# Kernel optimization log

Hardware: AMD Instinct MI355X
Metric: run time of the kernel (lower is better)

## Reference

```python
import jax, jax.numpy as jnp
import numpy as np

B, E, H, NC = 16384, 1024, 8, 32
FF = 4 * E

def _ln(x, g, b, eps=1e-5):
    m = jnp.mean(x, -1, keepdims=True)
    v = jnp.mean((x - m) ** 2, -1, keepdims=True)
    return (x - m) * jax.lax.rsqrt(v + eps) * g + b

def _mha1(q_in, kv_in, Wq, Wk, Wv, bq, bk, bv, Wo, bo):
    # seq_len == 1 for both query and key/value; x: [B, E]
    Bn = q_in.shape[0]
    dh = E // H
    q = (q_in @ Wq.T + bq).reshape(Bn, H, dh)
    k = (kv_in @ Wk.T + bk).reshape(Bn, H, dh)
    v = (kv_in @ Wv.T + bv).reshape(Bn, H, dh)
    s = jnp.sum(q * k, -1, keepdims=True) / np.float32(np.sqrt(dh))  # [B,H,1]
    w = jax.nn.softmax(s, axis=-1)  # single key -> weights == 1 exactly
    o = (w * v).reshape(Bn, E)
    return o @ Wo.T + bo

def _ffn(x, W1, b1, W2, b2):
    h = jax.nn.gelu(x @ W1.T + b1, approximate=False)  # torch GELU = exact erf
    return h @ W2.T + b2

def setup_inputs():
    key = jax.random.key(0)
    ks = iter(jax.random.split(key, 64))
    def w(shape, s=0.02):
        return jax.random.normal(next(ks), shape, jnp.float32) * s
    z = lambda n: jnp.zeros((n,), jnp.float32)
    o = lambda n: jnp.ones((n,), jnp.float32)
    d = {
        'lc_cls': jax.random.normal(next(ks), (B, E), jnp.float32),
        'tab_embedding': jax.random.normal(next(ks), (B, E), jnp.float32),
        'ln_lc_g': o(E), 'ln_lc_b': z(E),
        'ln_tab_g': o(E), 'ln_tab_b': z(E),
    }
    for p in ('alc', 'atab'):
        d[p + '_Wq'] = w((E, E)); d[p + '_Wk'] = w((E, E)); d[p + '_Wv'] = w((E, E))
        d[p + '_bq'] = z(E); d[p + '_bk'] = z(E); d[p + '_bv'] = z(E)
        d[p + '_Wo'] = w((E, E)); d[p + '_bo'] = z(E)
    for p in ('flc', 'ftab'):
        d[p + '_W1'] = w((FF, E)); d[p + '_b1'] = z(FF)
        d[p + '_W2'] = w((E, FF)); d[p + '_b2'] = z(E)
    d['on_g'] = o(2 * E); d['on_b'] = z(2 * E)
    d['c_W1'] = w((E, 2 * E)); d['c_b1'] = z(E)
    d['c_ln_g'] = o(E); d['c_ln_b'] = z(E)
    d['c_W2'] = w((NC, E)); d['c_b2'] = z(NC)
    return d

def reference(lc_cls, tab_embedding, ln_lc_g, ln_lc_b, ln_tab_g, ln_tab_b,
              alc_Wq, alc_Wk, alc_Wv, alc_bq, alc_bk, alc_bv, alc_Wo, alc_bo,
              atab_Wq, atab_Wk, atab_Wv, atab_bq, atab_bk, atab_bv, atab_Wo, atab_bo,
              flc_W1, flc_b1, flc_W2, flc_b2, ftab_W1, ftab_b1, ftab_W2, ftab_b2,
              on_g, on_b, c_W1, c_b1, c_ln_g, c_ln_b, c_W2, c_b2):
    # dropout is identity at inference
    lc_n = _ln(lc_cls, ln_lc_g, ln_lc_b)
    tab_n = _ln(tab_embedding, ln_tab_g, ln_tab_b)
    lc_cross = lc_cls + _mha1(lc_n, tab_n, alc_Wq, alc_Wk, alc_Wv, alc_bq, alc_bk, alc_bv, alc_Wo, alc_bo)
    tab_cross = tab_embedding + _mha1(tab_n, lc_n, atab_Wq, atab_Wk, atab_Wv, atab_bq, atab_bk, atab_bv, atab_Wo, atab_bo)
    lc_out = lc_cross + _ffn(lc_cross, flc_W1, flc_b1, flc_W2, flc_b2)
    tab_out = tab_cross + _ffn(tab_cross, ftab_W1, ftab_b1, ftab_W2, ftab_b2)
    fused = _ln(jnp.concatenate([lc_out, tab_out], axis=1), on_g, on_b)
    h = jax.nn.gelu(_ln(fused @ c_W1.T + c_b1, c_ln_g, c_ln_b), approximate=False)
    return h @ c_W2.T + c_b2
```

## Files before the change

kernel.cpp:

```cpp
#include <hip/hip_runtime.h>
#include <hip/hip_bf16.h>
#include <math.h>

typedef __bf16 bf16_t;
typedef __bf16 bf16x8 __attribute__((ext_vector_type(8)));
typedef __bf16 bf16x4 __attribute__((ext_vector_type(4)));
typedef float  f32x4  __attribute__((ext_vector_type(4)));

#define NB   16384
#define EDIM 1024
#define FFD  4096
#define NCD  32

__device__ __forceinline__ float gelu_exact(float x) {
    return 0.5f * x * (1.0f + erff(x * 0.70710678118654752f));
}

__device__ __forceinline__ void gload16(const bf16_t* g, bf16_t* l) {
    __builtin_amdgcn_global_load_lds(
        (__attribute__((address_space(1))) void*)(g),
        (__attribute__((address_space(3))) void*)(l),
        16, 0, 0);
}

#define PH_BAR() do { asm volatile("" ::: "memory"); \
                      __builtin_amdgcn_s_barrier();  \
                      asm volatile("" ::: "memory"); } while (0)

enum { EPI_PLAIN = 0, EPI_RESF32 = 1, EPI_GELU = 2, EPI_RESBF16 = 3 };

struct GemmArgs {
    const bf16_t* A0; const bf16_t* A1;
    const bf16_t* B0; const bf16_t* B1;
    const float*  bias0; const float* bias1;
    const void*   res0; const void*  res1;
    bf16_t*       out0; bf16_t*      out1;
};

template<int EPI>
__global__ __launch_bounds__(512, 4)
void gemmP2(GemmArgs g, int ldo, int co0, int co1, int M, int N, int K)
{
    __shared__ __align__(128) bf16_t lds[36864];
    char* const ldsb = (char*)lds;

    const int nx   = gridDim.x;
    const int ny   = M >> 8;
    const int nwg  = nx * gridDim.y;
    const int lin  = blockIdx.y * nx + blockIdx.x;
    const int Wx   = nwg >> 3;
    const int w    = (lin & 7) * Wx + (lin >> 3);
    const int perSide = nx * ny;
    const int side = w / perSide;
    const int r    = w - side * perSide;
    const int cg   = r / (ny << 3);
    const int tt   = r - cg * (ny << 3);
    const long bm  = (long)(tt >> 3) * 256;
    const long bn  = (long)((cg << 3) + (tt & 7)) * 128;

    const bf16_t* __restrict__ A    = side ? g.A1   : g.A0;
    const bf16_t* __restrict__ Bw   = side ? g.B1   : g.B0;
    const float*  __restrict__ bias = side ? g.bias1: g.bias0;
    const void*   __restrict__ resid= side ? g.res1 : g.res0;
    bf16_t*       __restrict__ out  = side ? g.out1 : g.out0;
    const int coloff = side ? co1 : co0;

    const int tid = threadIdx.x, lane = tid & 63, wave = tid >> 6;
    const int wm = wave >> 1, wn = wave & 1;
    const int fr = lane & 15, ks = lane >> 4;
    const int csw = ((ks ^ (fr & 3)) << 4);

    const int sl = ((tid & 3) ^ ((tid >> 2) & 3)) * 8;
    const bf16_t* gA = A  + (bm + (tid >> 2)) * (long)K + sl;
    const bf16_t* gB = Bw + (bn + (tid >> 2)) * (long)K + sl;
    bf16_t* const dA0 = (bf16_t*)(ldsb + wave * 1024);
    bf16_t* const dA1 = (bf16_t*)(ldsb + 8192  + wave * 1024);
    bf16_t* const dB  = (bf16_t*)(ldsb + 16384 + wave * 1024);

    const int nt = K >> 5;
    auto STAGE = [&](int t) {
        const int bufo = (t % 3) * 24576;
        const long kt = (long)t << 5;
        gload16(gA + kt,                 (bf16_t*)((char*)dA0 + bufo));
        gload16(gA + kt + 128 * (long)K, (bf16_t*)((char*)dA1 + bufo));
        gload16(gB + kt,                 (bf16_t*)((char*)dB  + bufo));
    };

    f32x4 acc[4][4] = {};

    STAGE(0);
    STAGE(1);
    asm volatile("s_waitcnt vmcnt(3)" ::: "memory");
    PH_BAR();

    for (int t = 0; t < nt; ++t) {
        const char* base = ldsb + (t % 3) * 24576;
        bf16x8 av[4], bv[4];
        #pragma unroll
        for (int i = 0; i < 4; ++i) {
            av[i] = *(const bf16x8*)(base + (wm * 64 + i * 16 + fr) * 64 + csw);
            bv[i] = *(const bf16x8*)(base + 16384 + (wn * 64 + i * 16 + fr) * 64 + csw);
        }
        if (t + 2 < nt) STAGE(t + 2);
        __builtin_amdgcn_s_setprio(1);
        #pragma unroll
        for (int mi = 0; mi < 4; ++mi)
            #pragma unroll
            for (int ni = 0; ni < 4; ++ni)
                acc[mi][ni] = __builtin_amdgcn_mfma_f32_16x16x32_bf16(
                                  av[mi], bv[ni], acc[mi][ni], 0, 0, 0);
        __builtin_amdgcn_s_setprio(0);
        if (t + 2 < nt) { asm volatile("s_waitcnt vmcnt(3)" ::: "memory"); }
        else            { asm volatile("s_waitcnt vmcnt(0)" ::: "memory"); }
        PH_BAR();
    }

    const int rq = (lane >> 4) * 4;
    #pragma unroll
    for (int mi = 0; mi < 4; ++mi) {
        #pragma unroll
        for (int ni = 0; ni < 4; ++ni) {
            const long n = bn + wn * 64 + ni * 16 + fr;
            const float bval = bias ? bias[n] : 0.0f;
            #pragma unroll
            for (int r2 = 0; r2 < 4; ++r2) {
                const long m = bm + wm * 64 + mi * 16 + rq + r2;
                float v = acc[mi][ni][r2] + bval;
                if (EPI == EPI_RESF32)  v += ((const float*)resid)[m * (long)N + n];
                if (EPI == EPI_RESBF16) v += (float)((const bf16_t*)resid)[m * (long)N + n];
                if (EPI == EPI_GELU)    v = gelu_exact(v);
                out[m * (long)ldo + coloff + n] = (bf16_t)v;
            }
        }
    }
}

__global__ __launch_bounds__(256)
void final_mfma(const bf16_t* __restrict__ U, const bf16_t* __restrict__ W2,
                const float* __restrict__ b2, float* __restrict__ out)
{
    __shared__ bf16_t sA[128 * 32];
    __shared__ bf16_t sB[32 * 32];
    const int tid = threadIdx.x, lane = tid & 63, wave = tid >> 6;
    const long bm = (long)blockIdx.x * 128;
    const int srow = lane >> 2, scol = (lane & 3) * 8;

    const bf16_t* gA = U + (bm + wave * 32 + srow) * (long)EDIM + scol;
    bf16_t* lA = sA + wave * 32 * 32;
    const bf16_t* gB = W2 + ((long)wave * 16 + srow) * EDIM + scol;
    bf16_t* lB = sB + wave * 16 * 32;

    const int fr = lane & 15, fk = (lane >> 4) * 8;
    const bf16_t* rA = sA + (wave * 32 + fr) * 32 + fk;
    const bf16_t* rB = sB + fr * 32 + fk;

    f32x4 acc[2][2] = {};
    for (int kt = 0; kt < EDIM; kt += 32) {
        gload16(gA + kt,             lA);
        gload16(gA + kt + 16 * EDIM, lA + 16 * 32);
        if (wave < 2) gload16(gB + kt, lB);
        __syncthreads();
        bf16x8 av[2], bv[2];
        av[0] = *(const bf16x8*)(rA);
        av[1] = *(const bf16x8*)(rA + 16 * 32);
        bv[0] = *(const bf16x8*)(rB);
        bv[1] = *(const bf16x8*)(rB + 16 * 32);
        #pragma unroll
        for (int mi = 0; mi < 2; ++mi)
            #pragma unroll
            for (int ni = 0; ni < 2; ++ni)
                acc[mi][ni] = __builtin_amdgcn_mfma_f32_16x16x32_bf16(
                                  av[mi], bv[ni], acc[mi][ni], 0, 0, 0);
        __syncthreads();
    }
    const int rq = (lane >> 4) * 4;
    #pragma unroll
    for (int mi = 0; mi < 2; ++mi)
        #pragma unroll
        for (int ni = 0; ni < 2; ++ni) {
            const int n = ni * 16 + fr;
            const float bval = b2[n];
            #pragma unroll
            for (int r = 0; r < 4; ++r) {
                const long m = bm + wave * 32 + mi * 16 + rq + r;
                out[m * NCD + n] = acc[mi][ni][r] + bval;
            }
        }
}

__global__ __launch_bounds__(256)
void ln_f32(const float* __restrict__ X, const float* __restrict__ g,
            const float* __restrict__ b, bf16_t* __restrict__ out)
{
    const long row = blockIdx.x;
    const int t = threadIdx.x;
    f32x4 x = ((const f32x4*)(X + row * EDIM))[t];
    float s = x[0] + x[1] + x[2] + x[3];
    float q = x[0]*x[0] + x[1]*x[1] + x[2]*x[2] + x[3]*x[3];
    #pragma unroll
    for (int off = 32; off; off >>= 1) { s += __shfl_xor(s, off); q += __shfl_xor(q, off); }
    __shared__ float red[8];
    if ((t & 63) == 0) { red[(t >> 6) * 2] = s; red[(t >> 6) * 2 + 1] = q; }
    __syncthreads();
    s = red[0] + red[2] + red[4] + red[6];
    q = red[1] + red[3] + red[5] + red[7];
    const float mean = s * (1.0f / EDIM);
    const float rs = rsqrtf(q * (1.0f / EDIM) - mean * mean + 1e-5f);
    f32x4 gg = ((const f32x4*)g)[t];
    f32x4 bb = ((const f32x4*)b)[t];
    bf16x4 o;
    #pragma unroll
    for (int j = 0; j < 4; ++j) o[j] = (bf16_t)((x[j] - mean) * rs * gg[j] + bb[j]);
    ((bf16x4*)(out + row * EDIM))[t] = o;
}

__global__ __launch_bounds__(256)
void ln_cat(const bf16_t* __restrict__ X, const float* __restrict__ g,
            const float* __restrict__ b, bf16_t* __restrict__ out)
{
    const long row = blockIdx.x;
    const int t = threadIdx.x;
    bf16x8 xv = ((const bf16x8*)(X + row * 2048))[t];
    float xf[8];
    float s = 0.f, q = 0.f;
    #pragma unroll
    for (int j = 0; j < 8; ++j) { xf[j] = (float)xv[j]; s += xf[j]; q += xf[j] * xf[j]; }
    #pragma unroll
    for (int off = 32; off; off >>= 1) { s += __shfl_xor(s, off); q += __shfl_xor(q, off); }
    __shared__ float red[8];
    if ((t & 63) == 0) { red[(t >> 6) * 2] = s; red[(t >> 6) * 2 + 1] = q; }
    __syncthreads();
    s = red[0] + red[2] + red[4] + red[6];
    q = red[1] + red[3] + red[5] + red[7];
    const float mean = s * (1.0f / 2048);
    const float rs = rsqrtf(q * (1.0f / 2048) - mean * mean + 1e-5f);
    f32x4 g0 = ((const f32x4*)g)[2 * t], g1 = ((const f32x4*)g)[2 * t + 1];
    f32x4 b0 = ((const f32x4*)b)[2 * t], b1 = ((const f32x4*)b)[2 * t + 1];
    bf16x8 o;
    #pragma unroll
    for (int j = 0; j < 4; ++j) o[j]     = (bf16_t)((xf[j]     - mean) * rs * g0[j] + b0[j]);
    #pragma unroll
    for (int j = 0; j < 4; ++j) o[4 + j] = (bf16_t)((xf[4 + j] - mean) * rs * g1[j] + b1[j]);
    ((bf16x8*)(out + row * 2048))[t] = o;
}

__global__ __launch_bounds__(256)
void ln_gelu(const bf16_t* __restrict__ X, const float* __restrict__ g,
             const float* __restrict__ b, bf16_t* __restrict__ out)
{
    const long row = blockIdx.x;
    const int t = threadIdx.x;
    bf16x4 xv = ((const bf16x4*)(X + row * EDIM))[t];
    float xf[4];
    float s = 0.f, q = 0.f;
    #pragma unroll
    for (int j = 0; j < 4; ++j) { xf[j] = (float)xv[j]; s += xf[j]; q += xf[j] * xf[j]; }
    #pragma unroll
    for (int off = 32; off; off >>= 1) { s += __shfl_xor(s, off); q += __shfl_xor(q, off); }
    __shared__ float red[8];
    if ((t & 63) == 0) { red[(t >> 6) * 2] = s; red[(t >> 6) * 2 + 1] = q; }
    __syncthreads();
    s = red[0] + red[2] + red[4] + red[6];
    q = red[1] + red[3] + red[5] + red[7];
    const float mean = s * (1.0f / EDIM);
    const float rs = rsqrtf(q * (1.0f / EDIM) - mean * mean + 1e-5f);
    f32x4 gg = ((const f32x4*)g)[t];
    f32x4 bb = ((const f32x4*)b)[t];
    bf16x4 o;
    #pragma unroll
    for (int j = 0; j < 4; ++j)
        o[j] = (bf16_t)gelu_exact((xf[j] - mean) * rs * gg[j] + bb[j]);
    ((bf16x4*)(out + row * EDIM))[t] = o;
}

__global__ void f2b(const float* __restrict__ in, bf16_t* __restrict__ out, long n4)
{
    long i = (long)blockIdx.x * blockDim.x + threadIdx.x;
    const long stride = (long)gridDim.x * blockDim.x;
    for (; i < n4; i += stride) {
        f32x4 v = ((const f32x4*)in)[i];
        bf16x4 o;
        #pragma unroll
        for (int j = 0; j < 4; ++j) o[j] = (bf16_t)v[j];
        ((bf16x4*)out)[i] = o;
    }
}

__global__ void tconv(const float* __restrict__ in, bf16_t* __restrict__ out)
{
    const long x = (long)blockIdx.x * 256 + threadIdx.x;
    const int k = (int)(x & (EDIM - 1));
    const int j = (int)(x >> 10);
    out[(long)j * EDIM + k] = (bf16_t)in[(long)k * EDIM + j];
}

__global__ __launch_bounds__(256)
void bcomb_k(const float* __restrict__ Wo, const float* __restrict__ bv,
             const float* __restrict__ bo, float* __restrict__ bc)
{
    const int i = blockIdx.x;
    const int t = threadIdx.x;
    f32x4 w = ((const f32x4*)(Wo + (long)i * EDIM))[t];
    f32x4 v = ((const f32x4*)bv)[t];
    float s = w[0]*v[0] + w[1]*v[1] + w[2]*v[2] + w[3]*v[3];
    #pragma unroll
    for (int off = 32; off; off >>= 1) s += __shfl_xor(s, off);
    __shared__ float red[4];
    if ((t & 63) == 0) red[t >> 6] = s;
    __syncthreads();
    if (t == 0) bc[i] = red[0] + red[1] + red[2] + red[3] + bo[i];
}

extern "C" void kernel_launch(void* const* d_in, const int* in_sizes, int n_in,
                              void* d_out, int out_size, void* d_ws, size_t ws_size,
                              hipStream_t stream)
{
    const float* lc_cls   = (const float*)d_in[0];
    const float* tab_emb  = (const float*)d_in[1];
    const float* ln_lc_g  = (const float*)d_in[2];
    const float* ln_lc_b  = (const float*)d_in[3];
    const float* ln_tab_g = (const float*)d_in[4];
    const float* ln_tab_b = (const float*)d_in[5];
    const float* alc_Wv   = (const float*)d_in[8];
    const float* alc_bv   = (const float*)d_in[11];
    const float* alc_Wo   = (const float*)d_in[12];
    const float* alc_bo   = (const float*)d_in[13];
    const float* atab_Wv  = (const float*)d_in[16];
    const float* atab_bv  = (const float*)d_in[19];
    const float* atab_Wo  = (const float*)d_in[20];
    const float* atab_bo  = (const float*)d_in[21];
    const float* flc_W1   = (const float*)d_in[22];
    const float* flc_b1   = (const float*)d_in[23];
    const float* flc_W2   = (const float*)d_in[24];
    const float* flc_b2   = (const float*)d_in[25];
    const float* ftab_W1  = (const float*)d_in[26];
    const float* ftab_b1  = (const float*)d_in[27];
    const float* ftab_W2  = (const float*)d_in[28];
    const float* ftab_b2  = (const float*)d_in[29];
    const float* on_g     = (const float*)d_in[30];
    const float* on_b     = (const float*)d_in[31];
    const float* c_W1     = (const float*)d_in[32];
    const float* c_b1     = (const float*)d_in[33];
    const float* c_ln_g   = (const float*)d_in[34];
    const float* c_ln_b   = (const float*)d_in[35];
    const float* c_W2     = (const float*)d_in[36];
    const float* c_b2     = (const float*)d_in[37];

    char* ws = (char*)d_ws;
    size_t woff = 0;
    auto walloc = [&](size_t bytes) {
        void* p = ws + woff;
        woff += (bytes + 255) & ~(size_t)255;
        return p;
    };
    bf16_t* Wc_lc  = (bf16_t*)walloc((size_t)EDIM * EDIM * 2);
    bf16_t* Wc_tab = (bf16_t*)walloc((size_t)EDIM * EDIM * 2);
    bf16_t* W1lc_b = (bf16_t*)walloc((size_t)FFD * EDIM * 2);
    bf16_t* W2lc_b = (bf16_t*)walloc((size_t)EDIM * FFD * 2);
    bf16_t* W1tab_b= (bf16_t*)walloc((size_t)FFD * EDIM * 2);
    bf16_t* W2tab_b= (bf16_t*)walloc((size_t)EDIM * FFD * 2);
    bf16_t* cW1_b  = (bf16_t*)walloc((size_t)EDIM * 2 * EDIM * 2);
    bf16_t* cW2_b  = (bf16_t*)walloc((size_t)NCD * EDIM * 2);
    float*  bc_lc  = (float*)walloc(EDIM * 4);
    float*  bc_tab = (float*)walloc(EDIM * 4);

    char* arena = ws + woff;
    const size_t arena_sz = (ws_size > woff) ? (ws_size - woff) : 0;

    int SB = NB;
    while (SB > 256 && (size_t)SB * 24576 > arena_sz) SB >>= 1;
    if ((size_t)SB * 24576 > arena_sz) return;

    const size_t S2 = (size_t)SB * 2048;
    bf16_t* lc_n  = (bf16_t*)(arena);
    bf16_t* tab_n = (bf16_t*)(arena + S2);
    bf16_t* cat   = (bf16_t*)(arena);
    bf16_t* lc_x  = (bf16_t*)(arena + 2 * S2);
    bf16_t* tab_x = (bf16_t*)(arena + 3 * S2);
    bf16_t* hbuf0 = (bf16_t*)(arena + 4 * S2);
    bf16_t* hbuf1 = (bf16_t*)(arena + 8 * S2);
    bf16_t* tbuf  = lc_x;
    bf16_t* ubuf  = tab_x;

    bf16_t* Wo_lc_b  = (bf16_t*)(arena);
    bf16_t* Wo_tab_b = (bf16_t*)(arena + (size_t)2 * 1024 * 1024);
    bf16_t* WvT_lc   = (bf16_t*)(arena + (size_t)4 * 1024 * 1024);
    bf16_t* WvT_tab  = (bf16_t*)(arena + (size_t)6 * 1024 * 1024);

    f2b<<<512, 256, 0, stream>>>(alc_Wo,  Wo_lc_b,  (long)EDIM * EDIM / 4);
    f2b<<<512, 256, 0, stream>>>(atab_Wo, Wo_tab_b, (long)EDIM * EDIM / 4);
    tconv<<<EDIM * EDIM / 256, 256, 0, stream>>>(alc_Wv,  WvT_lc);
    tconv<<<EDIM * EDIM / 256, 256, 0, stream>>>(atab_Wv, WvT_tab);
    f2b<<<2048, 256, 0, stream>>>(flc_W1,  W1lc_b,  (long)FFD * EDIM / 4);
    f2b<<<2048, 256, 0, stream>>>(flc_W2,  W2lc_b,  (long)EDIM * FFD / 4);
    f2b<<<2048, 256, 0, stream>>>(ftab_W1, W1tab_b, (long)FFD * EDIM / 4);
    f2b<<<2048, 256, 0, stream>>>(ftab_W2, W2tab_b, (long)EDIM * FFD / 4);
    f2b<<<1024, 256, 0, stream>>>(c_W1,    cW1_b,   (long)EDIM * 2 * EDIM / 4);
    f2b<<<32,   256, 0, stream>>>(c_W2,    cW2_b,   (long)NCD * EDIM / 4);
    bcomb_k<<<EDIM, 256, 0, stream>>>(alc_Wo,  alc_bv,  alc_bo,  bc_lc);
    bcomb_k<<<EDIM, 256, 0, stream>>>(atab_Wo, atab_bv, atab_bo, bc_tab);
    {
        GemmArgs ga = { Wo_lc_b, Wo_tab_b, WvT_lc, WvT_tab,
                        nullptr, nullptr, nullptr, nullptr, Wc_lc, Wc_tab };
        gemmP2<EPI_PLAIN><<<dim3(EDIM/128, (EDIM/256) * 2), 512, 0, stream>>>(
            ga, EDIM, 0, 0, EDIM, EDIM, EDIM);
    }

    for (long c0 = 0; c0 < NB; c0 += SB) {
        const float* lcI  = lc_cls  + c0 * EDIM;
        const float* tabI = tab_emb + c0 * EDIM;

        ln_f32<<<SB, 256, 0, stream>>>(lcI,  ln_lc_g,  ln_lc_b,  lc_n);
        ln_f32<<<SB, 256, 0, stream>>>(tabI, ln_tab_g, ln_tab_b, tab_n);

        {
            GemmArgs ga = { tab_n, lc_n, Wc_lc, Wc_tab, bc_lc, bc_tab,
                            lcI, tabI, lc_x, tab_x };
            gemmP2<EPI_RESF32><<<dim3(EDIM/128, (SB/256) * 2), 512, 0, stream>>>(
                ga, EDIM, 0, 0, SB, EDIM, EDIM);
        }
        {
            GemmArgs ga = { lc_x, tab_x, W1lc_b, W1tab_b, flc_b1, ftab_b1,
                            nullptr, nullptr, hbuf0, hbuf1 };
            gemmP2<EPI_GELU><<<dim3(FFD/128, (SB/256) * 2), 512, 0, stream>>>(
                ga, FFD, 0, 0, SB, FFD, EDIM);
        }
        {
            GemmArgs ga = { hbuf0, hbuf1, W2lc_b, W2tab_b, flc_b2, ftab_b2,
                            lc_x, tab_x, cat, cat };
            gemmP2<EPI_RESBF16><<<dim3(EDIM/128, (SB/256) * 2), 512, 0, stream>>>(
                ga, 2 * EDIM, 0, EDIM, SB, EDIM, FFD);
        }

        ln_cat<<<SB, 256, 0, stream>>>(cat, on_g, on_b, cat);

        {
            GemmArgs ga = { cat, cat, cW1_b, cW1_b, c_b1, c_b1,
                            nullptr, nullptr, tbuf, tbuf };
            gemmP2<EPI_PLAIN><<<dim3(EDIM/128, SB/256), 512, 0, stream>>>(
                ga, EDIM, 0, 0, SB, EDIM, 2 * EDIM);
        }
        ln_gelu<<<SB, 256, 0, stream>>>(tbuf, c_ln_g, c_ln_b, ubuf);
        final_mfma<<<SB / 128, 256, 0, stream>>>(ubuf, cW2_b, c_b2,
                                                 (float*)d_out + c0 * NCD);
    }
}
```

Measured before the change: 1.034 ms.

## Use 4-wave GEMM blocks with 128x64 per-wave tiles instead of 8 waves

The GEMM kernel now runs 256 threads (4 waves) per 256x128 block instead of 512. Each wave computes a 128x64 sub-tile with 8x4 MFMA accumulators, and each thread issues 6 global-to-LDS loads per stage instead of 3. The aim is more register-level reuse of the B fragments and fewer LDS reads per MFMA. The cost is higher VGPR pressure from doubling the accumulators, and fewer waves available to hide latency.

```diff
diff --git a/kernel.cpp b/kernel.cpp
--- a/kernel.cpp
+++ b/kernel.cpp
@@ -38,8 +38,8 @@
 };
 
 template<int EPI>
-__global__ __launch_bounds__(512, 4)
-void gemmP2(GemmArgs g, int ldo, int co0, int co1, int M, int N, int K)
+__global__ __launch_bounds__(256, 2)
+void gemmW(GemmArgs g, int ldo, int co0, int co1, int M, int N, int K)
 {
     __shared__ __align__(128) bf16_t lds[36864];
     char* const ldsb = (char*)lds;
@@ -73,58 +73,61 @@
     const int sl = ((tid & 3) ^ ((tid >> 2) & 3)) * 8;
     const bf16_t* gA = A  + (bm + (tid >> 2)) * (long)K + sl;
     const bf16_t* gB = Bw + (bn + (tid >> 2)) * (long)K + sl;
-    bf16_t* const dA0 = (bf16_t*)(ldsb + wave * 1024);
-    bf16_t* const dA1 = (bf16_t*)(ldsb + 8192  + wave * 1024);
-    bf16_t* const dB  = (bf16_t*)(ldsb + 16384 + wave * 1024);
 
     const int nt = K >> 5;
     auto STAGE = [&](int t) {
         const int bufo = (t % 3) * 24576;
         const long kt = (long)t << 5;
-        gload16(gA + kt,                 (bf16_t*)((char*)dA0 + bufo));
-        gload16(gA + kt + 128 * (long)K, (bf16_t*)((char*)dA1 + bufo));
-        gload16(gB + kt,                 (bf16_t*)((char*)dB  + bufo));
+        #pragma unroll
+        for (int i = 0; i < 4; ++i)
+            gload16(gA + kt + (long)i * 64 * K,
+                    (bf16_t*)(ldsb + bufo + i * 4096 + wave * 1024));
+        #pragma unroll
+        for (int i = 0; i < 2; ++i)
+            gload16(gB + kt + (long)i * 64 * K,
+                    (bf16_t*)(ldsb + bufo + 16384 + i * 4096 + wave * 1024));
     };
 
-    f32x4 acc[4][4] = {};
+    f32x4 acc[8][4] = {};
 
     STAGE(0);
     STAGE(1);
-    asm volatile("s_waitcnt vmcnt(3)" ::: "memory");
+    asm volatile("s_waitcnt vmcnt(6)" ::: "memory");
     PH_BAR();
 
     for (int t = 0; t < nt; ++t) {
         const char* base = ldsb + (t % 3) * 24576;
-        bf16x8 av[4], bv[4];
-        #pragma unroll
-        for (int i = 0; i < 4; ++i) {
-            av[i] = *(const bf16x8*)(base + (wm * 64 + i * 16 + fr) * 64 + csw);
+        bf16x8 av[8], bv[4];
+        #pragma unroll
+        for (int i = 0; i < 8; ++i)
+            av[i] = *(const bf16x8*)(base + (wm * 128 + i * 16 + fr) * 64 + csw);
+        #pragma unroll
+        for (int i = 0; i < 4; ++i)
             bv[i] = *(const bf16x8*)(base + 16384 + (wn * 64 + i * 16 + fr) * 64 + csw);
-        }
         if (t + 2 < nt) STAGE(t + 2);
         __builtin_amdgcn_s_setprio(1);
         #pragma unroll
-        for (int mi = 0; mi < 4; ++mi)
+        for (int mi = 0; mi < 8; ++mi)
             #pragma unroll
             for (int ni = 0; ni < 4; ++ni)
                 acc[mi][ni] = __builtin_amdgcn_mfma_f32_16x16x32_bf16(
                                   av[mi], bv[ni], acc[mi][ni], 0, 0, 0);
         __builtin_amdgcn_s_setprio(0);
-        if (t + 2 < nt) { asm volatile("s_waitcnt vmcnt(3)" ::: "memory"); }
+        if (t + 2 < nt) { asm volatile("s_waitcnt vmcnt(6)" ::: "memory"); }
         else            { asm volatile("s_waitcnt vmcnt(0)" ::: "memory"); }
         PH_BAR();
     }
 
     const int rq = (lane >> 4) * 4;
     #pragma unroll
-    for (int mi = 0; mi < 4; ++mi) {
+    for (int mi = 0; mi < 8; ++mi) {
         #pragma unroll
         for (int ni = 0; ni < 4; ++ni) {
             const long n = bn + wn * 64 + ni * 16 + fr;
             const float bval = bias ? bias[n] : 0.0f;
             #pragma unroll
             for (int r2 = 0; r2 < 4; ++r2) {
-                const long m = bm + wm * 64 + mi * 16 + rq + r2;
+                const long m = bm + wm * 128 + mi * 16 + rq + r2;
                 float v = acc[mi][ni][r2] + bval;
                 if (EPI == EPI_RESF32)  v += ((const float*)resid)[m * (long)N + n];
                 if (EPI == EPI_RESBF16) v += (float)((const bf16_t*)resid)[m * (long)N + n];
@@ -402,7 +405,7 @@
     {
         GemmArgs ga = { Wo_lc_b, Wo_tab_b, WvT_lc, WvT_tab,
                         nullptr, nullptr, nullptr, nullptr, Wc_lc, Wc_tab };
-        gemmP2<EPI_PLAIN><<<dim3(EDIM/128, (EDIM/256) * 2), 512, 0, stream>>>(
+        gemmW<EPI_PLAIN><<<dim3(EDIM/128, (EDIM/256) * 2), 256, 0, stream>>>(
             ga, EDIM, 0, 0, EDIM, EDIM, EDIM);
     }
 
@@ -416,19 +419,19 @@
         {
             GemmArgs ga = { tab_n, lc_n, Wc_lc, Wc_tab, bc_lc, bc_tab,
                             lcI, tabI, lc_x, tab_x };
-            gemmP2<EPI_RESF32><<<dim3(EDIM/128, (SB/256) * 2), 512, 0, stream>>>(
+            gemmW<EPI_RESF32><<<dim3(EDIM/128, (SB/256) * 2), 256, 0, stream>>>(
                 ga, EDIM, 0, 0, SB, EDIM, EDIM);
         }
         {
             GemmArgs ga = { lc_x, tab_x, W1lc_b, W1tab_b, flc_b1, ftab_b1,
                             nullptr, nullptr, hbuf0, hbuf1 };
-            gemmP2<EPI_GELU><<<dim3(FFD/128, (SB/256) * 2), 512, 0, stream>>>(
+            gemmW<EPI_GELU><<<dim3(FFD/128, (SB/256) * 2), 256, 0, stream>>>(
                 ga, FFD, 0, 0, SB, FFD, EDIM);
         }
         {
             GemmArgs ga = { hbuf0, hbuf1, W2lc_b, W2tab_b, flc_b2, ftab_b2,
                             lc_x, tab_x, cat, cat };
-            gemmP2<EPI_RESBF16><<<dim3(EDIM/128, (SB/256) * 2), 512, 0, stream>>>(
+            gemmW<EPI_RESBF16><<<dim3(EDIM/128, (SB/256) * 2), 256, 0, stream>>>(
                 ga, 2 * EDIM, 0, EDIM, SB, EDIM, FFD);
         }
 
@@ -437,7 +440,7 @@
         {
             GemmArgs ga = { cat, cat, cW1_b, cW1_b, c_b1, c_b1,
                             nullptr, nullptr, tbuf, tbuf };
-            gemmP2<EPI_PLAIN><<<dim3(EDIM/128, SB/256), 512, 0, stream>>>(
+            gemmW<EPI_PLAIN><<<dim3(EDIM/128, SB/256), 256, 0, stream>>>(
                 ga, EDIM, 0, 0, SB, EDIM, 2 * EDIM);
         }
         ln_gelu<<<SB, 256, 0, stream>>>(tbuf, c_ln_g, c_ln_b, ubuf);
```

After: 1.134 ms. 1.1x slower.
